# Kernel tuning notes

Measured on AMD Instinct MI355X. Metric: run time of the kernel, lower is better.

## Reference

```python
import jax, jax.numpy as jnp
import numpy as np

HIDDEN = 1024
N_HEAD = 16
HEAD_DIM = HIDDEN // N_HEAD


def setup_inputs() -> dict:
    key = jax.random.key(0)
    k1, k2, k3 = jax.random.split(key, 3)
    B, S = 4, 2048
    x = jax.random.normal(k1, (B, S, HIDDEN), dtype=jnp.float32)
    # nn.Linear(hidden, 3*hidden, bias=False): weight [3*hidden, hidden]
    w_qkv = jax.random.normal(k2, (3 * HIDDEN, HIDDEN), dtype=jnp.float32) * (HIDDEN ** -0.5)
    w_out = jax.random.normal(k3, (HIDDEN, HIDDEN), dtype=jnp.float32) * (HIDDEN ** -0.5)
    return {"x": x, "w_qkv": w_qkv, "w_out": w_out}


def _rope(q, k):
    # q, k: [B, H, S, D]
    S, D = q.shape[-2], q.shape[-1]
    pos = jnp.arange(S, dtype=jnp.float32)[:, None]          # [S, 1]
    ids = jnp.arange(D // 2, dtype=jnp.float32)              # [D/2]
    theta = jnp.power(jnp.float32(10000.0), 2.0 * ids / D)   # [D/2]
    ang = pos / theta                                        # [S, D/2]
    # torch code: sin at even slots, cos at odd slots; then repeat_interleave(2)
    sin = jnp.repeat(jnp.sin(ang), 2, axis=-1)               # [S, D]
    cos = jnp.repeat(jnp.cos(ang), 2, axis=-1)               # [S, D]

    def rot(t):
        # stack([-t_odd, t_even], -1).reshape -> interleaved rotate-half
        t2 = jnp.stack([-t[..., 1::2], t[..., 0::2]], axis=-1).reshape(t.shape)
        return t * cos + t2 * sin

    return rot(q), rot(k)


def reference(x, w_qkv, w_out):
    B, S, _ = x.shape
    qkv = jnp.einsum('bsd,ed->bse', x, w_qkv)                # [B, S, 3*hidden]
    qkv = qkv.reshape(B, S, N_HEAD, 3 * HEAD_DIM).transpose(0, 2, 1, 3)  # [B,H,S,3D]
    q, k, v = jnp.split(qkv, 3, axis=-1)                     # each [B,H,S,D]
    q, k = _rope(q, k)
    # NOTE: original forward never applies self.scale, mask (eval), or dropout.
    scores = jnp.einsum('bhqd,bhkd->bhqk', q, k)             # [B,H,S,S]
    probs = jax.nn.softmax(scores, axis=-1)
    out = jnp.einsum('bhqk,bhkd->bhqd', probs, v)            # [B,H,S,D]
    out = out.transpose(0, 2, 1, 3).reshape(B, S, HIDDEN)
    return jnp.einsum('bsd,ed->bse', out, w_out)
```

## Files before the change

### kernel.cpp

```cpp
#include <hip/hip_runtime.h>
#include <stdint.h>
#include <math.h>

#define NHEAD 16
#define HDIM 64
#define BATCH 4
#define SEQ 2048
#define NROWS (BATCH*SEQ)
#define LOG2E 1.4426950408889634f

typedef _Float16 f16x8 __attribute__((ext_vector_type(8)));
typedef _Float16 f16x4 __attribute__((ext_vector_type(4)));
typedef __fp16 h16x2 __attribute__((ext_vector_type(2)));
typedef float f32x4 __attribute__((ext_vector_type(4)));
typedef float f32x16 __attribute__((ext_vector_type(16)));
typedef unsigned int u32x4 __attribute__((ext_vector_type(4)));

typedef const __attribute__((address_space(1))) unsigned int* gas_ptr;
typedef __attribute__((address_space(3))) unsigned int* las_ptr;

__device__ __forceinline__ void gload_lds16(const void* g, void* l) {
  __builtin_amdgcn_global_load_lds((gas_ptr)g, (las_ptr)l, 16, 0, 0);
}

__device__ __forceinline__ float exp2_fast(float x) {
  float r; asm("v_exp_f32 %0, %1" : "=v"(r) : "v"(x)); return r;
}

__device__ __forceinline__ float max3f(float a, float b, float c) {
  float r; asm("v_max3_f32 %0, %1, %2, %3" : "=v"(r) : "v"(a), "v"(b), "v"(c)); return r;
}

__device__ __forceinline__ unsigned pku(float a, float b) {
  h16x2 p = __builtin_amdgcn_cvt_pkrtz(a, b);
  return __builtin_bit_cast(unsigned, p);
}

__global__ void cvt_f16_kernel(const float* __restrict__ in,
                               unsigned short* __restrict__ out, int n4) {
  int stride = gridDim.x * blockDim.x;
  for (int i = blockIdx.x * blockDim.x + threadIdx.x; i < n4; i += stride) {
    float4 v = ((const float4*)in)[i];
    f16x4 h;
    h[0] = (_Float16)v.x; h[1] = (_Float16)v.y;
    h[2] = (_Float16)v.z; h[3] = (_Float16)v.w;
    ((f16x4*)out)[i] = h;
  }
}

__global__ void sincos_kernel(float2* __restrict__ tab) {
  int idx = blockIdx.x * blockDim.x + threadIdx.x;
  int s = idx >> 5, i = idx & 31;
  float theta = powf(10000.0f, (float)i / 32.0f);
  float ang = (float)s / theta;
  tab[idx] = make_float2(sinf(ang), cosf(ang));
}

__global__ __launch_bounds__(256)
void gemm_qkv_f16(const unsigned short* __restrict__ A,
                  const unsigned short* __restrict__ B,
                  const float2* __restrict__ tab,
                  unsigned short* __restrict__ Qh,
                  unsigned short* __restrict__ Kh,
                  unsigned short* __restrict__ Vt) {
  const int K = 1024, nk = K >> 6;
  __shared__ unsigned short sA[2][128 * 64];
  __shared__ unsigned short sB[2][128 * 64];
  const int tid = threadIdx.x;
  const int lane = tid & 63;
  const int wave = tid >> 6;
  const int wr = wave >> 1, wc = wave & 1;
  const long m0 = (long)blockIdx.x * 128;
  const long n0 = (long)blockIdx.y * 128;

  f32x4 acc[4][4] = {};

  auto stage = [&](int buf, int kt) {
    const long k0 = (long)kt * 64;
    const char* Ab = (const char*)A;
    const char* Bb = (const char*)B;
#pragma unroll
    for (int qd = 0; qd < 4; ++qd) {
      int o = qd * 4096 + tid * 16;
      int row = o >> 7;
      int colb = (((o >> 4) & 7) ^ (row & 7)) << 4;
      gload_lds16(Ab + ((m0 + row) * K + k0) * 2 + colb, (char*)&sA[buf][0] + o);
      gload_lds16(Bb + ((n0 + row) * K + k0) * 2 + colb, (char*)&sB[buf][0] + o);
    }
  };

  const int lhi = lane >> 4, llo = lane & 15;
  const int rA = wr * 64 + llo;
  const int rB = wc * 64 + llo;
  int chsw[2];
#pragma unroll
  for (int s = 0; s < 2; ++s) chsw[s] = (((s * 4 + lhi) ^ (llo & 7)) << 3);

  stage(0, 0);
  __syncthreads();
  int cur = 0;

  for (int kt = 0; kt < nk; ++kt) {
    if (kt + 1 < nk) stage(cur ^ 1, kt + 1);
    f16x8 af[2][4], bfr[2][4];
#pragma unroll
    for (int s = 0; s < 2; ++s)
#pragma unroll
      for (int m = 0; m < 4; ++m)
        af[s][m] = *(const f16x8*)&sA[cur][(rA + m * 16) * 64 + chsw[s]];
#pragma unroll
    for (int s = 0; s < 2; ++s)
#pragma unroll
      for (int n = 0; n < 4; ++n)
        bfr[s][n] = *(const f16x8*)&sB[cur][(rB + n * 16) * 64 + chsw[s]];
#pragma unroll
    for (int m = 0; m < 4; ++m)
#pragma unroll
      for (int n = 0; n < 4; ++n) {
        acc[m][n] = __builtin_amdgcn_mfma_f32_16x16x32_f16(af[0][m], bfr[0][n], acc[m][n], 0, 0, 0);
        acc[m][n] = __builtin_amdgcn_mfma_f32_16x16x32_f16(af[1][m], bfr[1][n], acc[m][n], 0, 0, 0);
      }
    __syncthreads();
    cur ^= 1;
  }

  const int rb0 = (int)m0 + wr * 64 + lhi * 4;
  const int bidx = rb0 >> 11;
  const int s0 = rb0 & 2047;
#pragma unroll
  for (int n = 0; n < 4; ++n) {
    const int col = (int)n0 + wc * 64 + llo + n * 16;
    const int h = col / 192;
    const int off = col - h * 192;
    const int part = off >> 6;
    const int d = off & 63;
    const long bh_ = (long)(bidx * 16 + h);
    if (part < 2) {
      _Float16* dst = (_Float16*)(part == 0 ? Qh : Kh) + bh_ * SEQ * 64 + d;
      const float qs = (part == 0) ? LOG2E : 1.0f;
      const float2* tp = tab + (d >> 1);
      const int sgn = d & 1;
#pragma unroll
      for (int m = 0; m < 4; ++m)
#pragma unroll
        for (int r = 0; r < 4; ++r) {
          int s = s0 + m * 16 + r;
          float v = acc[m][n][r];
          float p = __shfl_xor(v, 1, 64);
          float2 sc = tp[s * 32];
          float rot = sgn ? (v * sc.y + p * sc.x) : (v * sc.y - p * sc.x);
          dst[(long)s * 64] = (_Float16)(rot * qs);
        }
    } else {
      _Float16* dst = (_Float16*)Vt + (bh_ * 64 + d) * SEQ;
#pragma unroll
      for (int m = 0; m < 4; ++m)
#pragma unroll
        for (int r = 0; r < 4; ++r)
          dst[s0 + m * 16 + r] = (_Float16)acc[m][n][r];
    }
  }
}

__global__ __launch_bounds__(512, 4)
void attn_kernel(const unsigned short* __restrict__ Qh,
                 const unsigned short* __restrict__ Kh,
                 const unsigned short* __restrict__ Vt,
                 unsigned short* __restrict__ AOut) {
  __shared__ unsigned short sK[4][64 * 64];
  __shared__ unsigned short sV[4][64 * 64];

  const int NT = SEQ / 64;
  const int tid = threadIdx.x;
  const int w = tid >> 6, lane = tid & 63;
  const int q32 = lane & 31, hi = lane >> 5;

  const int bid = blockIdx.x;
  const int xcd = bid & 7, rest = bid >> 3;
  const int bh = (rest >> 3) * 8 + xcd;
  const int qt = rest & 7;
  const int b = bh >> 4, h = bh & 15;
  const int q = qt * 256 + w * 32 + q32;

  f16x8 aq[4];
#pragma unroll
  for (int ds = 0; ds < 4; ++ds)
    aq[ds] = *(const f16x8*)&Qh[((long)bh * SEQ + q) * 64 + ds * 16 + hi * 8];

  f32x16 acc0 = {}, acc1 = {};
  float mrow = -INFINITY, lrow = 0.f;

  const int r7 = q32 & 7;
  int off[2][4];
#pragma unroll
  for (int t = 0; t < 2; ++t)
#pragma unroll
    for (int s = 0; s < 4; ++s)
      off[t][s] = (t * 32 + q32) * 64 + (((s * 2 + hi) ^ r7) << 3);

  const int cr = tid >> 3, cp = tid & 7, cps = cp ^ (cr & 7);
  const long kSrc0 = ((long)bh * SEQ + cr) * 64 + cps * 8;
  const long vSrc0 = ((long)bh * 64 + cr) * SEQ + cps * 8;

  auto stage = [&](int buf, int kt) {
    gload_lds16(&Kh[kSrc0 + (long)kt * 4096], (char*)&sK[buf][0] + tid * 16);
    gload_lds16(&Vt[vSrc0 + (long)kt * 64],   (char*)&sV[buf][0] + tid * 16);
  };

#define MKPA(dst, S, R0) {                                        \
    unsigned A0 = pku(S[R0 + 0], S[R0 + 1]);                      \
    unsigned A1 = pku(S[R0 + 2], S[R0 + 3]);                      \
    unsigned B0 = pku(S[R0 + 4], S[R0 + 5]);                      \
    unsigned B1 = pku(S[R0 + 6], S[R0 + 7]);                      \
    asm("v_permlane32_swap_b32 %0, %1" : "+v"(A0), "+v"(B0));     \
    asm("v_permlane32_swap_b32 %0, %1" : "+v"(A1), "+v"(B1));     \
    u32x4 tt; tt[0] = A0; tt[1] = A1; tt[2] = B0; tt[3] = B1;     \
    dst = __builtin_bit_cast(f16x8, tt); }

  auto tile = [&](int t) {
    const unsigned short* Kb = &sK[t & 3][0];
    const unsigned short* Vb = &sV[t & 3][0];

    f32x16 s0v = {}, s1v = {};
    __builtin_amdgcn_s_setprio(1);
#pragma unroll
    for (int ds = 0; ds < 4; ++ds) {
      f16x8 k0 = *(const f16x8*)&Kb[off[0][ds]];
      f16x8 k1 = *(const f16x8*)&Kb[off[1][ds]];
      s0v = __builtin_amdgcn_mfma_f32_32x32x16_f16(k0, aq[ds], s0v, 0, 0, 0);
      s1v = __builtin_amdgcn_mfma_f32_32x32x16_f16(k1, aq[ds], s1v, 0, 0, 0);
    }
    __builtin_amdgcn_s_setprio(0);

    float t0 = max3f(s0v[0], s0v[1], s0v[2]);
    float t1 = max3f(s0v[3], s0v[4], s0v[5]);
    float t2 = max3f(s0v[6], s0v[7], s0v[8]);
    float t3 = max3f(s0v[9], s0v[10], s0v[11]);
    float t4 = max3f(s0v[12], s0v[13], s0v[14]);
    float t5 = max3f(s0v[15], s1v[0], s1v[1]);
    float t6 = max3f(s1v[2], s1v[3], s1v[4]);
    float t7 = max3f(s1v[5], s1v[6], s1v[7]);
    float t8 = max3f(s1v[8], s1v[9], s1v[10]);
    float t9 = max3f(s1v[11], s1v[12], s1v[13]);
    float t10 = fmaxf(s1v[14], s1v[15]);
    float u0 = max3f(t0, t1, t2);
    float u1 = max3f(t3, t4, t5);
    float u2 = max3f(t6, t7, t8);
    float u3 = fmaxf(t9, t10);
    float tmax = fmaxf(max3f(u0, u1, u2), u3);
    tmax = fmaxf(tmax, __shfl_xor(tmax, 32, 64));

    if (__any(tmax > mrow + 8.0f)) {
      float mnew = fmaxf(mrow, tmax);
      float al = exp2_fast(mrow - mnew);
      mrow = mnew;
#pragma unroll
      for (int r = 0; r < 16; ++r) { acc0[r] *= al; acc1[r] *= al; }
      lrow *= al;
    }
    const float mr = mrow;

#pragma unroll
    for (int r = 0; r < 16; ++r) {
      s0v[r] = exp2_fast(s0v[r] - mr);
      s1v[r] = exp2_fast(s1v[r] - mr);
    }

    float sa[16];
#pragma unroll
    for (int r = 0; r < 16; ++r) sa[r] = s0v[r] + s1v[r];
#pragma unroll
    for (int d = 8; d > 0; d >>= 1)
#pragma unroll
      for (int r = 0; r < d; ++r) sa[r] = sa[r] + sa[r + d];
    lrow += sa[0] + __shfl_xor(sa[0], 32, 64);

    f16x8 pa[4];
    MKPA(pa[0], s0v, 0);
    MKPA(pa[1], s0v, 8);
    MKPA(pa[2], s1v, 0);
    MKPA(pa[3], s1v, 8);

    __builtin_amdgcn_s_setprio(1);
#pragma unroll
    for (int ks = 0; ks < 4; ++ks) {
      f16x8 v0 = *(const f16x8*)&Vb[off[0][ks]];
      f16x8 v1 = *(const f16x8*)&Vb[off[1][ks]];
      acc0 = __builtin_amdgcn_mfma_f32_32x32x16_f16(v0, pa[ks], acc0, 0, 0, 0);
      acc1 = __builtin_amdgcn_mfma_f32_32x32x16_f16(v1, pa[ks], acc1, 0, 0, 0);
    }
    __builtin_amdgcn_s_setprio(0);
  };

  stage(0, 0); stage(1, 1);
  __syncthreads();

  for (int it = 0; it < NT / 2; ++it) {
    const int t0 = it * 2;
    if (it + 1 < NT / 2) { stage((t0 + 2) & 3, t0 + 2); stage((t0 + 3) & 3, t0 + 3); }
    tile(t0);
    tile(t0 + 1);
    __syncthreads();
  }

  float inv = 1.f / lrow;
  const long obase = ((long)b * SEQ + q) * 1024 + h * 64;
#define EPI(ACCV, DT)                                              \
  {                                                                \
    _Pragma("unroll")                                              \
    for (int rg = 0; rg < 4; ++rg) {                               \
      f16x4 o;                                                     \
      _Pragma("unroll")                                            \
      for (int e = 0; e < 4; ++e)                                  \
        o[e] = (_Float16)(ACCV[rg * 4 + e] * inv);                 \
      *(f16x4*)&AOut[obase + DT * 32 + rg * 8 + hi * 4] = o;       \
    }                                                              \
  }
  EPI(acc0, 0);
  EPI(acc1, 1);
}

__global__ __launch_bounds__(256)
void gemm_out_f16(const unsigned short* __restrict__ A,
                  const unsigned short* __restrict__ B,
                  float* __restrict__ C, int M, int N, int K) {
  __shared__ unsigned short sA[2][128 * 64];
  __shared__ unsigned short sB[2][128 * 64];
  const int tid = threadIdx.x;
  const int lane = tid & 63;
  const int wave = tid >> 6;
  const int wr = wave >> 1, wc = wave & 1;
  const long m0 = (long)blockIdx.x * 128;
  const long n0 = (long)blockIdx.y * 128;

  f32x4 acc[4][4] = {};

  auto stage = [&](int buf, int kt) {
    const long k0 = (long)kt * 64;
    const char* Ab = (const char*)A;
    const char* Bb = (const char*)B;
#pragma unroll
    for (int qd = 0; qd < 4; ++qd) {
      int o = qd * 4096 + tid * 16;
      int row = o >> 7;
      int colb = (((o >> 4) & 7) ^ (row & 7)) << 4;
      gload_lds16(Ab + ((m0 + row) * K + k0) * 2 + colb, (char*)&sA[buf][0] + o);
      gload_lds16(Bb + ((n0 + row) * K + k0) * 2 + colb, (char*)&sB[buf][0] + o);
    }
  };

  const int lhi = lane >> 4, llo = lane & 15;
  const int rA = wr * 64 + llo;
  const int rB = wc * 64 + llo;
  int chsw[2];
#pragma unroll
  for (int s = 0; s < 2; ++s) chsw[s] = (((s * 4 + lhi) ^ (llo & 7)) << 3);

  const int nk = K >> 6;
  stage(0, 0);
  __syncthreads();
  int cur = 0;

  for (int kt = 0; kt < nk; ++kt) {
    if (kt + 1 < nk) stage(cur ^ 1, kt + 1);
    f16x8 af[2][4], bfr[2][4];
#pragma unroll
    for (int s = 0; s < 2; ++s)
#pragma unroll
      for (int m = 0; m < 4; ++m)
        af[s][m] = *(const f16x8*)&sA[cur][(rA + m * 16) * 64 + chsw[s]];
#pragma unroll
    for (int s = 0; s < 2; ++s)
#pragma unroll
      for (int n = 0; n < 4; ++n)
        bfr[s][n] = *(const f16x8*)&sB[cur][(rB + n * 16) * 64 + chsw[s]];
#pragma unroll
    for (int m = 0; m < 4; ++m)
#pragma unroll
      for (int n = 0; n < 4; ++n) {
        acc[m][n] = __builtin_amdgcn_mfma_f32_16x16x32_f16(af[0][m], bfr[0][n], acc[m][n], 0, 0, 0);
        acc[m][n] = __builtin_amdgcn_mfma_f32_16x16x32_f16(af[1][m], bfr[1][n], acc[m][n], 0, 0, 0);
      }
    __syncthreads();
    cur ^= 1;
  }

  const long rbase = m0 + wr * 64 + lhi * 4;
#pragma unroll
  for (int n = 0; n < 4; ++n) {
    const long col = n0 + wc * 64 + llo + n * 16;
#pragma unroll
    for (int m = 0; m < 4; ++m)
#pragma unroll
      for (int r = 0; r < 4; ++r)
        C[(rbase + m * 16 + r) * N + col] = acc[m][n][r];
  }
}

extern "C" void kernel_launch(void* const* d_in, const int* in_sizes, int n_in,
                              void* d_out, int out_size, void* d_ws, size_t ws_size,
                              hipStream_t stream) {
  const float* x     = (const float*)d_in[0];
  const float* w_qkv = (const float*)d_in[1];
  const float* w_out = (const float*)d_in[2];
  float* out = (float*)d_out;
  char* ws = (char*)d_ws;

  unsigned short* xb    = (unsigned short*)(ws + 0);
  unsigned short* attnb = xb;
  unsigned short* wqkvb = (unsigned short*)(ws + 16777216);
  unsigned short* woutb = (unsigned short*)(ws + 23068672);
  unsigned short* Qh    = (unsigned short*)(ws + 25165824);
  unsigned short* Kh    = (unsigned short*)(ws + 41943040);
  unsigned short* Vt    = (unsigned short*)(ws + 58720256);
  float2*         tab   = (float2*)(ws + 75497472);

  cvt_f16_kernel<<<2048, 256, 0, stream>>>(x, xb, NROWS * 1024 / 4);
  cvt_f16_kernel<<<1024, 256, 0, stream>>>(w_qkv, wqkvb, 3072 * 1024 / 4);
  cvt_f16_kernel<<<512, 256, 0, stream>>>(w_out, woutb, 1024 * 1024 / 4);
  sincos_kernel<<<SEQ * 32 / 256, 256, 0, stream>>>(tab);

  gemm_qkv_f16<<<dim3(64, 24), 256, 0, stream>>>(xb, wqkvb, tab, Qh, Kh, Vt);
  attn_kernel<<<512, 512, 0, stream>>>(Qh, Kh, Vt, attnb);
  gemm_out_f16<<<dim3(64, 8), 256, 0, stream>>>(attnb, woutb, out, NROWS, 1024, 1024);
}
```

Before: 205.1 us.

## Fuse prep kernels, compute softmax row sum via MFMA, use permlane max

Merges the three f16 conversion launches and the sincos table launch into one prep kernel, which removes launch overhead. In attention, the per-row softmax denominator is now produced by an extra MFMA against a vector of ones instead of a VALU reduction plus a shuffle. The cross-half max reduction uses v_permlane32_swap instead of a shuffle. The extra MFMA adds matrix-core work per tile to save VALU adds and cross-lane traffic.

```diff
diff --git a/kernel.cpp b/kernel.cpp
--- a/kernel.cpp
+++ b/kernel.cpp
@@ -36,24 +36,44 @@
   return __builtin_bit_cast(unsigned, p);
 }
 
-__global__ void cvt_f16_kernel(const float* __restrict__ in,
-                               unsigned short* __restrict__ out, int n4) {
-  int stride = gridDim.x * blockDim.x;
-  for (int i = blockIdx.x * blockDim.x + threadIdx.x; i < n4; i += stride) {
-    float4 v = ((const float4*)in)[i];
+__device__ __forceinline__ float xhalf_max(float a) {
+  float b;
+  asm volatile("v_mov_b32 %0, %1" : "=v"(b) : "v"(a));
+  asm volatile("v_permlane32_swap_b32 %0, %1" : "+v"(a), "+v"(b));
+  return fmaxf(a, b);
+}
+
+__global__ void prep_kernel(const float* __restrict__ x,
+                            const float* __restrict__ wq,
+                            const float* __restrict__ wo,
+                            unsigned short* __restrict__ xb,
+                            unsigned short* __restrict__ wqb,
+                            unsigned short* __restrict__ wob,
+                            float2* __restrict__ tab) {
+  const int idx = blockIdx.x * blockDim.x + threadIdx.x;
+  const int stride = gridDim.x * blockDim.x;
+  const int NS = SEQ * 32;
+  const int N1 = NROWS * 1024 / 4;
+  const int N2 = 3072 * 1024 / 4;
+  const int N3 = 1024 * 1024 / 4;
+
+  if (idx < NS) {
+    int s = idx >> 5, j = idx & 31;
+    float theta = powf(10000.0f, (float)j / 32.0f);
+    float ang = (float)s / theta;
+    tab[idx] = make_float2(sinf(ang), cosf(ang));
+  }
+  for (int i = idx; i < N1 + N2 + N3; i += stride) {
+    const float* src; unsigned short* dst; int k;
+    if (i < N1)            { src = x;  dst = xb;  k = i; }
+    else if (i < N1 + N2)  { src = wq; dst = wqb; k = i - N1; }
+    else                   { src = wo; dst = wob; k = i - N1 - N2; }
+    float4 v = ((const float4*)src)[k];
     f16x4 h;
     h[0] = (_Float16)v.x; h[1] = (_Float16)v.y;
     h[2] = (_Float16)v.z; h[3] = (_Float16)v.w;
-    ((f16x4*)out)[i] = h;
-  }
-}
-
-__global__ void sincos_kernel(float2* __restrict__ tab) {
-  int idx = blockIdx.x * blockDim.x + threadIdx.x;
-  int s = idx >> 5, i = idx & 31;
-  float theta = powf(10000.0f, (float)i / 32.0f);
-  float ang = (float)s / theta;
-  tab[idx] = make_float2(sinf(ang), cosf(ang));
+    ((f16x4*)dst)[k] = h;
+  }
 }
 
 __global__ __launch_bounds__(256)
@@ -187,8 +207,8 @@
   for (int ds = 0; ds < 4; ++ds)
     aq[ds] = *(const f16x8*)&Qh[((long)bh * SEQ + q) * 64 + ds * 16 + hi * 8];
 
-  f32x16 acc0 = {}, acc1 = {};
-  float mrow = -INFINITY, lrow = 0.f;
+  f32x16 acc0 = {}, acc1 = {}, accl = {};
+  float mrow = -INFINITY;
 
   const int r7 = q32 & 7;
   int off[2][4];
@@ -206,6 +226,10 @@
     gload_lds16(&Kh[kSrc0 + (long)kt * 4096], (char*)&sK[buf][0] + tid * 16);
     gload_lds16(&Vt[vSrc0 + (long)kt * 64],   (char*)&sV[buf][0] + tid * 16);
   };
+
+  f16x8 vones;
+#pragma unroll
+  for (int j = 0; j < 8; ++j) vones[j] = (_Float16)1.0f;
 
 #define MKPA(dst, S, R0) {                                        \
     unsigned A0 = pku(S[R0 + 0], S[R0 + 1]);                      \
@@ -247,16 +271,14 @@
     float u1 = max3f(t3, t4, t5);
     float u2 = max3f(t6, t7, t8);
     float u3 = fmaxf(t9, t10);
-    float tmax = fmaxf(max3f(u0, u1, u2), u3);
-    tmax = fmaxf(tmax, __shfl_xor(tmax, 32, 64));
+    float tmax = xhalf_max(fmaxf(max3f(u0, u1, u2), u3));
 
     if (__any(tmax > mrow + 8.0f)) {
       float mnew = fmaxf(mrow, tmax);
       float al = exp2_fast(mrow - mnew);
       mrow = mnew;
 #pragma unroll
-      for (int r = 0; r < 16; ++r) { acc0[r] *= al; acc1[r] *= al; }
-      lrow *= al;
+      for (int r = 0; r < 16; ++r) { acc0[r] *= al; acc1[r] *= al; accl[r] *= al; }
     }
     const float mr = mrow;
 
@@ -265,15 +287,6 @@
       s0v[r] = exp2_fast(s0v[r] - mr);
       s1v[r] = exp2_fast(s1v[r] - mr);
     }
-
-    float sa[16];
-#pragma unroll
-    for (int r = 0; r < 16; ++r) sa[r] = s0v[r] + s1v[r];
-#pragma unroll
-    for (int d = 8; d > 0; d >>= 1)
-#pragma unroll
-      for (int r = 0; r < d; ++r) sa[r] = sa[r] + sa[r + d];
-    lrow += sa[0] + __shfl_xor(sa[0], 32, 64);
 
     f16x8 pa[4];
     MKPA(pa[0], s0v, 0);
@@ -288,6 +301,7 @@
       f16x8 v1 = *(const f16x8*)&Vb[off[1][ks]];
       acc0 = __builtin_amdgcn_mfma_f32_32x32x16_f16(v0, pa[ks], acc0, 0, 0, 0);
       acc1 = __builtin_amdgcn_mfma_f32_32x32x16_f16(v1, pa[ks], acc1, 0, 0, 0);
+      accl = __builtin_amdgcn_mfma_f32_32x32x16_f16(vones, pa[ks], accl, 0, 0, 0);
     }
     __builtin_amdgcn_s_setprio(0);
   };
@@ -303,7 +317,7 @@
     __syncthreads();
   }
 
-  float inv = 1.f / lrow;
+  float inv = 1.f / accl[0];
   const long obase = ((long)b * SEQ + q) * 1024 + h * 64;
 #define EPI(ACCV, DT)                                              \
   {                                                                \
@@ -415,11 +429,7 @@
   unsigned short* Vt    = (unsigned short*)(ws + 58720256);
   float2*         tab   = (float2*)(ws + 75497472);
 
-  cvt_f16_kernel<<<2048, 256, 0, stream>>>(x, xb, NROWS * 1024 / 4);
-  cvt_f16_kernel<<<1024, 256, 0, stream>>>(w_qkv, wqkvb, 3072 * 1024 / 4);
-  cvt_f16_kernel<<<512, 256, 0, stream>>>(w_out, woutb, 1024 * 1024 / 4);
-  sincos_kernel<<<SEQ * 32 / 256, 256, 0, stream>>>(tab);
-
+  prep_kernel<<<2048, 256, 0, stream>>>(x, w_qkv, w_out, xb, wqkvb, woutb, tab);
   gemm_qkv_f16<<<dim3(64, 24), 256, 0, stream>>>(xb, wqkvb, tab, Qh, Kh, Vt);
   attn_kernel<<<512, 512, 0, stream>>>(Qh, Kh, Vt, attnb);
   gemm_out_f16<<<dim3(64, 8), 256, 0, stream>>>(attnb, woutb, out, NROWS, 1024, 1024);
```

Result: faster. 200.1 us (-2.4%).
